# Optimization experiments

Measured on AMD Instinct MI355X. Metric: run time of the kernel, lower is better.

## Reference

```python
import jax, jax.numpy as jnp
import numpy as np

N_NODES = 100000
HIDDEN = 128
N_EDGES = 1000000


def setup_inputs() -> dict:
    key = jax.random.key(0)
    k1, k2, k3 = jax.random.split(key, 3)
    z = jax.random.normal(k1, (N_NODES, HIDDEN), dtype=jnp.float32)
    edge_index = jax.random.randint(k2, (2, N_EDGES), 0, N_NODES, dtype=jnp.int64)
    # xavier_uniform for square matrix: bound = sqrt(6/(fan_in+fan_out))
    bound = float(np.sqrt(6.0 / (HIDDEN + HIDDEN)))
    weights = jax.random.uniform(k3, (HIDDEN, HIDDEN), dtype=jnp.float32,
                                 minval=-bound, maxval=bound)
    return {"z": z, "edge_index": edge_index, "weights": weights}


def reference(z, edge_index, weights):
    # symm=True: symmetrize the bilinear form
    W = weights + weights.T                      # [d, d]
    z_src = z[edge_index[0]]                     # [E, d] gather
    z_dst = z[edge_index[1]]                     # [E, d] gather
    # torch: (W @ z_dst.T).T == z_dst @ W.T
    value = jnp.einsum('ed,dk,ek->e', z_src, W, z_dst)  # row-wise bilinear score
    return jax.nn.sigmoid(value)
```

## Files before the change

### kernel.cpp

```cpp
#include <hip/hip_runtime.h>

#define HIDDEN 128
#define BSHIFT 10
#define NBMAX 128
#define CAP 10752
#define OVF_MAX 65536

typedef _Float16 f16;
typedef f16 f16x2 __attribute__((ext_vector_type(2)));
typedef f16 f16x8 __attribute__((ext_vector_type(8)));
typedef float f32x16 __attribute__((ext_vector_type(16)));
typedef unsigned long long ull;
typedef ull ull2 __attribute__((ext_vector_type(2)));

static __device__ __forceinline__ float fdot2(f16x2 a, f16x2 b, float c) {
    return __builtin_amdgcn_fdot2(a, b, c, false);
}

__global__ __launch_bounds__(256) void prep_w(const float* __restrict__ w,
                                              f16* __restrict__ wsh_t,
                                              int* __restrict__ cursor,
                                              int* __restrict__ ovf_cnt) {
    int idx = blockIdx.x * 256 + threadIdx.x;
    if (idx < NBMAX) cursor[idx] = idx * CAP;
    if (idx == NBMAX) ovf_cnt[0] = 0;
    int n = idx >> 7, k = idx & 127;
    wsh_t[idx] = (f16)(w[k * HIDDEN + n] + w[n * HIDDEN + k]);
}

__global__ __launch_bounds__(256) void gemm_scatter(const float* __restrict__ z,
                                                    const f16* __restrict__ wsh_t,
                                                    f16* __restrict__ zh,
                                                    f16* __restrict__ uh,
                                                    const int* __restrict__ eidx,
                                                    int* __restrict__ cursor,
                                                    ull* __restrict__ perm,
                                                    ull* __restrict__ ovf,
                                                    int* __restrict__ ovf_cnt,
                                                    int nrows, int E, int nb, int ngemm) {
    __shared__ f16 wlt[HIDDEN * HIDDEN];
    int tid = threadIdx.x;

    if (blockIdx.x >= ngemm) {
        int* lh    = (int*)wlt;
        int* lbase = lh + NBMAX;
        int* lrank = lbase + NBMAX;
        int base = (blockIdx.x - ngemm) * 4096;
        if (tid < NBMAX) { lh[tid] = 0; lrank[tid] = 0; }
        __syncthreads();
        int s[16], d[16], bb[16];
        #pragma unroll
        for (int i = 0; i < 16; ++i) {
            int e = base + i * 256 + tid;
            bb[i] = -1;
            if (e < E) {
                s[i] = eidx[e]; d[i] = eidx[E + e];
                bb[i] = d[i] >> BSHIFT;
                atomicAdd(&lh[bb[i]], 1);
            }
        }
        __syncthreads();
        if (tid < nb && lh[tid]) lbase[tid] = atomicAdd(&cursor[tid], lh[tid]);
        __syncthreads();
        #pragma unroll
        for (int i = 0; i < 16; ++i) {
            if (bb[i] >= 0) {
                int e = base + i * 256 + tid;
                int r = atomicAdd(&lrank[bb[i]], 1);
                long pos = (long)lbase[bb[i]] + r;
                ull v = (ull)s[i] | ((ull)d[i] << 17) | ((ull)(e + 1) << 34);
                if (pos < (long)(bb[i] + 1) * CAP) perm[pos] = v;
                else {
                    int o = atomicAdd(ovf_cnt, 1);
                    if (o < OVF_MAX) ovf[o] = v;
                }
            }
        }
        return;
    }

    {
        const f16x8* g = (const f16x8*)wsh_t;
        #pragma unroll
        for (int it = 0; it < 8; ++it) {
            int idx = it * 256 + tid;
            int j = idx >> 4, kc = idx & 15;
            *(f16x8*)&wlt[j * HIDDEN + (((kc + (j & 7)) & 15) << 3)] = g[idx];
        }
    }
    __syncthreads();

    int wave = tid >> 6, lane = tid & 63;
    int row0 = blockIdx.x * 128 + wave * 32;
    if (row0 > nrows - 32) row0 = nrows - 32;

    int m = lane & 31, half = lane >> 5;
    int rot = m & 7;
    const float* zr = z  + (size_t)(row0 + m) * HIDDEN + half * 8;
    f16*        zhr = zh + (size_t)(row0 + m) * HIDDEN + half * 8;
    const f16* wrow = &wlt[m * HIDDEN];

    f32x16 acc0, acc1, acc2, acc3;
    #pragma unroll
    for (int r = 0; r < 16; ++r) { acc0[r] = 0.f; acc1[r] = 0.f; acc2[r] = 0.f; acc3[r] = 0.f; }

    #pragma unroll
    for (int ks = 0; ks < 8; ++ks) {
        float4 a0 = *(const float4*)(zr + 16 * ks);
        float4 a1 = *(const float4*)(zr + 16 * ks + 4);
        f16x8 af = {(f16)a0.x, (f16)a0.y, (f16)a0.z, (f16)a0.w,
                    (f16)a1.x, (f16)a1.y, (f16)a1.z, (f16)a1.w};
        *(f16x8*)(zhr + 16 * ks) = af;
        int c = ((half + 2 * ks + rot) & 15) << 3;
        f16x8 b0 = *(const f16x8*)&wrow[c];
        f16x8 b1 = *(const f16x8*)&wrow[32 * HIDDEN + c];
        f16x8 b2 = *(const f16x8*)&wrow[64 * HIDDEN + c];
        f16x8 b3 = *(const f16x8*)&wrow[96 * HIDDEN + c];
        acc0 = __builtin_amdgcn_mfma_f32_32x32x16_f16(af, b0, acc0, 0, 0, 0);
        acc1 = __builtin_amdgcn_mfma_f32_32x32x16_f16(af, b1, acc1, 0, 0, 0);
        acc2 = __builtin_amdgcn_mfma_f32_32x32x16_f16(af, b2, acc2, 0, 0, 0);
        acc3 = __builtin_amdgcn_mfma_f32_32x32x16_f16(af, b3, acc3, 0, 0, 0);
    }

    f16* ur = uh + (size_t)row0 * HIDDEN;
    #pragma unroll
    for (int r = 0; r < 16; ++r) {
        int row = (r & 3) + 8 * (r >> 2) + 4 * half;
        f16* p = ur + (size_t)row * HIDDEN + m;
        p[0]  = (f16)acc0[r];
        p[32] = (f16)acc1[r];
        p[64] = (f16)acc2[r];
        p[96] = (f16)acc3[r];
    }
}

static __device__ __forceinline__ void score_edge(const f16* uh, const f16* zh,
                                                  ull p, float* out, int t, int E) {
    int src = (int)(p & 0x1FFFF);
    int dst = (int)((p >> 17) & 0x1FFFF);
    int ep  = (int)(p >> 34);
    const float4* a4 = (const float4*)(uh + (size_t)src * HIDDEN);
    const float4* b4 = (const float4*)(zh + (size_t)dst * HIDDEN);
    float4 av = a4[t], bv = b4[t];
    const f16x2* ap = (const f16x2*)&av;
    const f16x2* bp = (const f16x2*)&bv;
    float s = 0.f;
    #pragma unroll
    for (int i = 0; i < 4; ++i) s = fdot2(ap[i], bp[i], s);
    #pragma unroll
    for (int off = 8; off > 0; off >>= 1) s += __shfl_down(s, off, 16);
    if (t == 0 && ep > 0 && ep <= E) out[ep - 1] = 1.0f / (1.0f + __expf(-s));
}

__global__ __launch_bounds__(256, 8) void edge_bin(const f16* __restrict__ uh,
                                                   const f16* __restrict__ zh,
                                                   const ull* __restrict__ perm,
                                                   const ull* __restrict__ ovf,
                                                   const int* __restrict__ ovf_cnt,
                                                   float* __restrict__ out,
                                                   int E, int cpx, int nmain) {
    int tid = threadIdx.x;
    int g = tid >> 4, t = tid & 15;
    int b = blockIdx.x;
    if (b >= nmain) {
        int n = ovf_cnt[0];
        if (n > OVF_MAX) n = OVF_MAX;
        for (int i = (b - nmain) * 16 + g; i < n; i += 32 * 16)
            score_edge(uh, zh, ovf[i], out, t, E);
        return;
    }
    int chunk = (b & 7) * cpx + (b >> 3);
    long slot = (long)chunk * 32 + g * 2;
    ull2 p = *(const ull2*)&perm[slot];

    int src0 = (int)(p.x & 0x1FFFF), dst0 = (int)((p.x >> 17) & 0x1FFFF), e0 = (int)(p.x >> 34);
    int src1 = (int)(p.y & 0x1FFFF), dst1 = (int)((p.y >> 17) & 0x1FFFF), e1 = (int)(p.y >> 34);

    float4 a0 = ((const float4*)(uh + (size_t)src0 * HIDDEN))[t];
    float4 b0 = ((const float4*)(zh + (size_t)dst0 * HIDDEN))[t];
    float4 a1 = ((const float4*)(uh + (size_t)src1 * HIDDEN))[t];
    float4 b1 = ((const float4*)(zh + (size_t)dst1 * HIDDEN))[t];

    const f16x2* ap0 = (const f16x2*)&a0; const f16x2* bp0 = (const f16x2*)&b0;
    const f16x2* ap1 = (const f16x2*)&a1; const f16x2* bp1 = (const f16x2*)&b1;
    float s0 = 0.f, s1 = 0.f;
    #pragma unroll
    for (int i = 0; i < 4; ++i) {
        s0 = fdot2(ap0[i], bp0[i], s0);
        s1 = fdot2(ap1[i], bp1[i], s1);
    }
    #pragma unroll
    for (int off = 8; off > 0; off >>= 1) {
        s0 += __shfl_xor(s0, off, 16);
        s1 += __shfl_xor(s1, off, 16);
    }
    float sv = (t == 0) ? s0 : s1;
    int   ev = (t == 0) ? e0 : e1;
    if (t < 2 && ev > 0 && ev <= E) out[ev - 1] = 1.0f / (1.0f + __expf(-sv));
}

__global__ __launch_bounds__(256) void edge_score16(const f16* __restrict__ uh,
                                                    const f16* __restrict__ zh,
                                                    const int* __restrict__ eidx,
                                                    float* __restrict__ out, int E) {
    int tid = threadIdx.x;
    int g = tid >> 4, t = tid & 15;
    int e = blockIdx.x * 16 + g;
    if (e >= E) return;
    ull p = (ull)eidx[e] | ((ull)eidx[E + e] << 17) | ((ull)(e + 1) << 34);
    score_edge(uh, zh, p, out, t, E);
}

extern "C" void kernel_launch(void* const* d_in, const int* in_sizes, int n_in,
                              void* d_out, int out_size, void* d_ws, size_t ws_size,
                              hipStream_t stream) {
    const float* z    = (const float*)d_in[0];
    const int*   eidx = (const int*)d_in[1];
    const float* w    = (const float*)d_in[2];
    float* out = (float*)d_out;

    int nrows = in_sizes[0] / HIDDEN;
    int E = out_size;
    int nb = (nrows >> BSHIFT) + 1;

    f16* wsh_t  = (f16*)d_ws;
    f16* zh     = wsh_t + HIDDEN * HIDDEN;
    f16* uh     = zh + (size_t)nrows * HIDDEN;
    int* cursor = (int*)(uh + (size_t)nrows * HIDDEN);
    int* ovf_cnt = cursor + NBMAX;
    ull* ovf    = (ull*)(ovf_cnt + 4);
    ull* perm   = ovf + OVF_MAX;

    long nslots = (long)nb * CAP;
    size_t need = (size_t)((char*)(perm + nslots) - (char*)d_ws);
    bool binned = ws_size >= need;

    int ngemm = (nrows + 127) / 128;
    int nscat = (E + 4095) / 4096;

    prep_w<<<64, 256, 0, stream>>>(w, wsh_t, cursor, ovf_cnt);
    if (binned) {
        gemm_scatter<<<ngemm + nscat, 256, 0, stream>>>(z, wsh_t, zh, uh, eidx, cursor,
                                                        perm, ovf, ovf_cnt, nrows, E, nb, ngemm);
        long ngrp = nslots / 32;
        int cpx = (int)(ngrp / 8);
        int nmain = (int)ngrp;
        edge_bin<<<nmain + 32, 256, 0, stream>>>(uh, zh, perm, ovf, ovf_cnt, out, E, cpx, nmain);
    } else {
        gemm_scatter<<<ngemm, 256, 0, stream>>>(z, wsh_t, zh, uh, eidx, cursor,
                                                perm, ovf, ovf_cnt, nrows, E, nb, ngemm);
        edge_score16<<<(E + 15) / 16, 256, 0, stream>>>(uh, zh, eidx, out, E);
    }
}
```

Baseline: 157.1 us.

## Stage z tiles through LDS with coalesced loads and process two row tiles per block

The GEMM path now loads z in coalesced float4 chunks by the whole block, converts them to fp16, writes zh and a swizzled LDS tile, then feeds MFMA from LDS in two K halves. Each block handles 256 rows (two 128-row tiles), halving the GEMM grid so the W staging into LDS is amortised over more rows. This replaces strided per-lane global reads of z. It costs an extra 16KB of LDS, which may lower occupancy, and adds block barriers.

```diff
diff --git a/kernel.cpp b/kernel.cpp
--- a/kernel.cpp
+++ b/kernel.cpp
@@ -8,6 +8,7 @@
 
 typedef _Float16 f16;
 typedef f16 f16x2 __attribute__((ext_vector_type(2)));
+typedef f16 f16x4 __attribute__((ext_vector_type(4)));
 typedef f16 f16x8 __attribute__((ext_vector_type(8)));
 typedef float f32x16 __attribute__((ext_vector_type(16)));
 typedef unsigned long long ull;
@@ -39,6 +40,7 @@
                                                     int* __restrict__ ovf_cnt,
                                                     int nrows, int E, int nb, int ngemm) {
     __shared__ f16 wlt[HIDDEN * HIDDEN];
+    __shared__ f16 zla[128 * 64];
     int tid = threadIdx.x;
 
     if (blockIdx.x >= ngemm) {
@@ -88,49 +90,69 @@
             *(f16x8*)&wlt[j * HIDDEN + (((kc + (j & 7)) & 15) << 3)] = g[idx];
         }
     }
-    __syncthreads();
 
     int wave = tid >> 6, lane = tid & 63;
-    int row0 = blockIdx.x * 128 + wave * 32;
-    if (row0 > nrows - 32) row0 = nrows - 32;
-
     int m = lane & 31, half = lane >> 5;
     int rot = m & 7;
-    const float* zr = z  + (size_t)(row0 + m) * HIDDEN + half * 8;
-    f16*        zhr = zh + (size_t)(row0 + m) * HIDDEN + half * 8;
+    int blk0 = blockIdx.x * 256;
     const f16* wrow = &wlt[m * HIDDEN];
 
-    f32x16 acc0, acc1, acc2, acc3;
-    #pragma unroll
-    for (int r = 0; r < 16; ++r) { acc0[r] = 0.f; acc1[r] = 0.f; acc2[r] = 0.f; acc3[r] = 0.f; }
-
-    #pragma unroll
-    for (int ks = 0; ks < 8; ++ks) {
-        float4 a0 = *(const float4*)(zr + 16 * ks);
-        float4 a1 = *(const float4*)(zr + 16 * ks + 4);
-        f16x8 af = {(f16)a0.x, (f16)a0.y, (f16)a0.z, (f16)a0.w,
-                    (f16)a1.x, (f16)a1.y, (f16)a1.z, (f16)a1.w};
-        *(f16x8*)(zhr + 16 * ks) = af;
-        int c = ((half + 2 * ks + rot) & 15) << 3;
-        f16x8 b0 = *(const f16x8*)&wrow[c];
-        f16x8 b1 = *(const f16x8*)&wrow[32 * HIDDEN + c];
-        f16x8 b2 = *(const f16x8*)&wrow[64 * HIDDEN + c];
-        f16x8 b3 = *(const f16x8*)&wrow[96 * HIDDEN + c];
-        acc0 = __builtin_amdgcn_mfma_f32_32x32x16_f16(af, b0, acc0, 0, 0, 0);
-        acc1 = __builtin_amdgcn_mfma_f32_32x32x16_f16(af, b1, acc1, 0, 0, 0);
-        acc2 = __builtin_amdgcn_mfma_f32_32x32x16_f16(af, b2, acc2, 0, 0, 0);
-        acc3 = __builtin_amdgcn_mfma_f32_32x32x16_f16(af, b3, acc3, 0, 0, 0);
-    }
-
-    f16* ur = uh + (size_t)row0 * HIDDEN;
-    #pragma unroll
-    for (int r = 0; r < 16; ++r) {
-        int row = (r & 3) + 8 * (r >> 2) + 4 * half;
-        f16* p = ur + (size_t)row * HIDDEN + m;
-        p[0]  = (f16)acc0[r];
-        p[32] = (f16)acc1[r];
-        p[64] = (f16)acc2[r];
-        p[96] = (f16)acc3[r];
+    #pragma unroll
+    for (int t = 0; t < 2; ++t) {
+        int srow = blk0 + t * 128;
+        int row0 = srow + wave * 32;
+        if (row0 > nrows - 32) row0 = nrows - 32;
+
+        f32x16 acc0, acc1, acc2, acc3;
+        #pragma unroll
+        for (int r = 0; r < 16; ++r) { acc0[r] = 0.f; acc1[r] = 0.f; acc2[r] = 0.f; acc3[r] = 0.f; }
+
+        int lbase = (row0 - srow + m) * 64;
+
+        #pragma unroll
+        for (int h = 0; h < 2; ++h) {
+            {
+                #pragma unroll
+                for (int it = 0; it < 8; ++it) {
+                    int idx = it * 256 + tid;
+                    int j = idx >> 4, c4 = idx & 15;
+                    int jrow = srow + j;
+                    int jc = jrow < nrows ? jrow : nrows - 1;
+                    float4 zv = *(const float4*)(z + (size_t)jc * HIDDEN + h * 64 + c4 * 4);
+                    f16x4 v = {(f16)zv.x, (f16)zv.y, (f16)zv.z, (f16)zv.w};
+                    if (jrow < nrows)
+                        *(f16x4*)(zh + (size_t)jrow * HIDDEN + h * 64 + c4 * 4) = v;
+                    *(f16x4*)&zla[j * 64 + ((((c4 >> 1) + (j & 7)) & 7) << 3) + (c4 & 1) * 4] = v;
+                }
+            }
+            __syncthreads();
+            #pragma unroll
+            for (int kp = 0; kp < 4; ++kp) {
+                f16x8 af = *(const f16x8*)&zla[lbase + (((half + 2 * kp + rot) & 7) << 3)];
+                int ks = h * 4 + kp;
+                int c = ((half + 2 * ks + rot) & 15) << 3;
+                f16x8 b0 = *(const f16x8*)&wrow[c];
+                f16x8 b1 = *(const f16x8*)&wrow[32 * HIDDEN + c];
+                f16x8 b2 = *(const f16x8*)&wrow[64 * HIDDEN + c];
+                f16x8 b3 = *(const f16x8*)&wrow[96 * HIDDEN + c];
+                acc0 = __builtin_amdgcn_mfma_f32_32x32x16_f16(af, b0, acc0, 0, 0, 0);
+                acc1 = __builtin_amdgcn_mfma_f32_32x32x16_f16(af, b1, acc1, 0, 0, 0);
+                acc2 = __builtin_amdgcn_mfma_f32_32x32x16_f16(af, b2, acc2, 0, 0, 0);
+                acc3 = __builtin_amdgcn_mfma_f32_32x32x16_f16(af, b3, acc3, 0, 0, 0);
+            }
+            __syncthreads();
+        }
+
+        f16* ur = uh + (size_t)row0 * HIDDEN;
+        #pragma unroll
+        for (int r = 0; r < 16; ++r) {
+            int row = (r & 3) + 8 * (r >> 2) + 4 * half;
+            f16* p = ur + (size_t)row * HIDDEN + m;
+            p[0]  = (f16)acc0[r];
+            p[32] = (f16)acc1[r];
+            p[64] = (f16)acc2[r];
+            p[96] = (f16)acc3[r];
+        }
     }
 }
 
@@ -235,7 +257,7 @@
     size_t need = (size_t)((char*)(perm + nslots) - (char*)d_ws);
     bool binned = ws_size >= need;
 
-    int ngemm = (nrows + 127) / 128;
+    int ngemm = (nrows + 255) / 256;
     int nscat = (E + 4095) / 4096;
 
     prep_w<<<64, 256, 0, stream>>>(w, wsh_t, cursor, ovf_cnt);
```

Result: slower. 171.7 us (+9.3%).
